# Optimization experiments

Hardware: AMD Instinct MI355X
Metric: run time of the kernel (lower is better)

The kernel has to match this reference:

```python
import jax, jax.numpy as jnp
import numpy as np

D_MODEL = 768
NUM_HEADS = 12
DEPTH = D_MODEL // NUM_HEADS


def setup_inputs() -> dict:
    key = jax.random.key(0)
    ks = jax.random.split(key, 11)
    B, S, D = 2, 2048, D_MODEL
    scale = 1.0 / np.sqrt(D)
    inp = {
        "v": jax.random.normal(ks[0], (B, S, D), jnp.float32),
        "k": jax.random.normal(ks[1], (B, S, D), jnp.float32),
        "q": jax.random.normal(ks[2], (B, S, D), jnp.float32),
        "wq": jax.random.normal(ks[3], (D, D), jnp.float32) * scale,
        "bq": jnp.zeros((D,), jnp.float32),
        "wk": jax.random.normal(ks[4], (D, D), jnp.float32) * scale,
        "bk": jnp.zeros((D,), jnp.float32),
        "wv": jax.random.normal(ks[5], (D, D), jnp.float32) * scale,
        "bv": jnp.zeros((D,), jnp.float32),
        "wo": jax.random.normal(ks[6], (D, D), jnp.float32) * scale,
        "bo": jnp.zeros((D,), jnp.float32),
    }
    return inp


def _split_heads(x):
    # (B, S, D) -> (B, H, S, depth)
    B, S, _ = x.shape
    return x.reshape(B, S, NUM_HEADS, DEPTH).transpose(0, 2, 1, 3)


def reference(v, k, q, wq, bq, wk, bk, wv, bv, wo, bo):
    B, S, D = q.shape
    qh = _split_heads(q @ wq + bq)  # (B,H,S,dh)
    kh = _split_heads(k @ wk + bk)
    vh = _split_heads(v @ wv + bv)
    logits = jnp.einsum("bhqd,bhkd->bhqk", qh, kh) / jnp.sqrt(
        jnp.asarray(DEPTH, qh.dtype)
    )
    attn = jax.nn.softmax(logits, axis=-1)  # (B,H,S,S)
    ctx = jnp.einsum("bhqk,bhkd->bhqd", attn, vh)
    ctx = ctx.transpose(0, 2, 1, 3).reshape(B, S, D)
    return ctx @ wo + bo
```

## Files before the change

kernel.cpp:

```cpp
#include <hip/hip_runtime.h>
#include <hip/hip_bf16.h>
#include <math.h>

typedef __bf16 bf16;
typedef __attribute__((ext_vector_type(8))) __bf16 bf16x8;
typedef __attribute__((ext_vector_type(4))) __bf16 bf16x4v;
typedef __attribute__((ext_vector_type(4))) float f32x4;

#define MFMA16(a, b, c) __builtin_amdgcn_mfma_f32_16x16x32_bf16(a, b, c, 0, 0, 0)

__device__ __forceinline__ void gld16(const bf16* g, bf16* l) {
  __builtin_amdgcn_global_load_lds((const __attribute__((address_space(1))) void*)g,
                                   (__attribute__((address_space(3))) void*)l, 16, 0, 0);
}

__global__ __launch_bounds__(256) void prep(const float* __restrict__ q,
                                            const float* __restrict__ k,
                                            const float* __restrict__ v,
                                            bf16* __restrict__ qb, bf16* __restrict__ kb,
                                            bf16* __restrict__ vb,
                                            const float* __restrict__ w0,
                                            const float* __restrict__ w1,
                                            const float* __restrict__ w2,
                                            const float* __restrict__ w3,
                                            bf16* __restrict__ t0, bf16* __restrict__ t1,
                                            bf16* __restrict__ t2, bf16* __restrict__ t3) {
  const int lin = blockIdx.x;
  if (lin < 4608) {
    const int which = lin / 1536, idx = lin % 1536;
    const float* a = which == 0 ? q : (which == 1 ? k : v);
    bf16* o = which == 0 ? qb : (which == 1 ? kb : vb);
    const size_t i = ((size_t)idx * 256 + threadIdx.x) * 8;
    const float4 f0 = *(const float4*)(a + i);
    const float4 f1 = *(const float4*)(a + i + 4);
    bf16x8 r = {(bf16)f0.x, (bf16)f0.y, (bf16)f0.z, (bf16)f0.w,
                (bf16)f1.x, (bf16)f1.y, (bf16)f1.z, (bf16)f1.w};
    *(bf16x8*)(o + i) = r;
  } else {
    const int w = lin - 4608;
    const int z = w / 576, rem = w % 576;
    const int by = rem / 24, bx = rem % 24;
    const float* W = z == 0 ? w0 : (z == 1 ? w1 : (z == 2 ? w2 : w3));
    bf16* T = z == 0 ? t0 : (z == 1 ? t1 : (z == 2 ? t2 : t3));
    __shared__ float t[32][33];
    const int tx = threadIdx.x & 31, ty = threadIdx.x >> 5;
    const int c0 = bx * 32, r0 = by * 32;
#pragma unroll
    for (int i = 0; i < 4; ++i) {
      const int r = ty + 8 * i;
      t[r][tx] = W[(size_t)(r0 + r) * 768 + c0 + tx];
    }
    __syncthreads();
#pragma unroll
    for (int i = 0; i < 4; ++i) {
      const int r = ty + 8 * i;
      T[(size_t)(c0 + r) * 768 + r0 + tx] = (bf16)t[tx][r];
    }
  }
}

__device__ __forceinline__ void gemm_core(const bf16* __restrict__ A, const bf16* __restrict__ BT,
                                          int row0, int col0, bf16* As, bf16* Bs,
                                          f32x4 acc[4][4]) {
  const int tid = threadIdx.x;
  const int lane = tid & 63, wave = tid >> 6;
  const int m15 = lane & 15, kg = lane >> 4;
  const int wm = wave >> 1, wn = wave & 1;
  const int pr16 = lane & 15;
  const int pk8 = (lane >> 4) * 8;
#pragma unroll
  for (int i = 0; i < 4; ++i)
#pragma unroll
    for (int j = 0; j < 4; ++j) acc[i][j] = f32x4{0.f, 0.f, 0.f, 0.f};

  for (int k0 = 0; k0 < 768; k0 += 32) {
#pragma unroll
    for (int j = 0; j < 2; ++j) {
      const int i = wave * 2 + j;
      gld16(A + (size_t)(row0 + 16 * i + pr16) * 768 + k0 + pk8, As + i * 512);
      gld16(BT + (size_t)(col0 + 16 * i + pr16) * 768 + k0 + pk8, Bs + i * 512);
    }
    __syncthreads();
    bf16x8 af[4], bfr[4];
#pragma unroll
    for (int t = 0; t < 4; ++t)
      af[t] = *(const bf16x8*)(As + (4 * wm + t) * 512 + kg * 128 + m15 * 8);
#pragma unroll
    for (int t = 0; t < 4; ++t)
      bfr[t] = *(const bf16x8*)(Bs + (4 * wn + t) * 512 + kg * 128 + m15 * 8);
#pragma unroll
    for (int mt = 0; mt < 4; ++mt)
#pragma unroll
      for (int nt = 0; nt < 4; ++nt) acc[mt][nt] = MFMA16(af[mt], bfr[nt], acc[mt][nt]);
    __syncthreads();
  }
}

__global__ __launch_bounds__(256, 3) void gemm_qkv(
    const bf16* __restrict__ qb, const bf16* __restrict__ kb, const bf16* __restrict__ vb,
    const bf16* __restrict__ wqT, const bf16* __restrict__ wkT, const bf16* __restrict__ wvT,
    const float* __restrict__ bq, const float* __restrict__ bk, const float* __restrict__ bv,
    bf16* __restrict__ Qh, bf16* __restrict__ Kh, bf16* __restrict__ Vt) {
  __shared__ bf16 As[128 * 32], Bs[128 * 32];
  const bf16 *A, *BT;
  const float* bias;
  bf16* out;
  int mode;
  if (blockIdx.z == 0) { A = qb; BT = wqT; bias = bq; out = Qh; mode = 0; }
  else if (blockIdx.z == 1) { A = kb; BT = wkT; bias = bk; out = Kh; mode = 0; }
  else { A = vb; BT = wvT; bias = bv; out = Vt; mode = 1; }
  const int row0 = blockIdx.y * 128, col0 = blockIdx.x * 128;
  f32x4 acc[4][4];
  gemm_core(A, BT, row0, col0, As, Bs, acc);

  const int lane = threadIdx.x & 63, wave = threadIdx.x >> 6;
  const int m15 = lane & 15, kg = lane >> 4;
  const int wm = wave >> 1, wn = wave & 1;
#pragma unroll
  for (int mt = 0; mt < 4; ++mt) {
#pragma unroll
    for (int nt = 0; nt < 4; ++nt) {
      const int col = col0 + 64 * wn + 16 * nt + m15;
      const float bb = bias[col];
      const int h = col >> 6, d = col & 63;
      const int rowb = row0 + 64 * wm + 16 * mt + kg * 4;
      const int b = rowb >> 11, s0 = rowb & 2047;
      if (mode == 0) {
#pragma unroll
        for (int r = 0; r < 4; ++r)
          out[((size_t)(b * 12 + h) * 2048 + s0 + r) * 64 + d] = (bf16)(acc[mt][nt][r] + bb);
      } else {
        bf16x4v pk;
#pragma unroll
        for (int r = 0; r < 4; ++r) pk[r] = (bf16)(acc[mt][nt][r] + bb);
        *(bf16x4v*)&out[((size_t)(b * 12 + h) * 64 + d) * 2048 + s0] = pk;
      }
    }
  }
}

__global__ __launch_bounds__(256, 3) void gemm_out(const bf16* __restrict__ A,
                                                   const bf16* __restrict__ BT,
                                                   const float* __restrict__ bias,
                                                   float* __restrict__ out) {
  __shared__ bf16 As[64 * 32], Bs[64 * 32];
  const int tid = threadIdx.x;
  const int lane = tid & 63, wave = tid >> 6;
  const int m15 = lane & 15, kg = lane >> 4;
  const int wm = wave >> 1, wn = wave & 1;
  const int row0 = blockIdx.y * 64, col0 = blockIdx.x * 64;
  const int pr16 = lane & 15, pk8 = (lane >> 4) * 8;

  f32x4 acc[2][2];
#pragma unroll
  for (int i = 0; i < 2; ++i)
#pragma unroll
    for (int j = 0; j < 2; ++j) acc[i][j] = f32x4{0.f, 0.f, 0.f, 0.f};

  for (int k0 = 0; k0 < 768; k0 += 32) {
    gld16(A + (size_t)(row0 + 16 * wave + pr16) * 768 + k0 + pk8, As + wave * 512);
    gld16(BT + (size_t)(col0 + 16 * wave + pr16) * 768 + k0 + pk8, Bs + wave * 512);
    __syncthreads();
    bf16x8 af[2], bfr[2];
#pragma unroll
    for (int t = 0; t < 2; ++t)
      af[t] = *(const bf16x8*)(As + (2 * wm + t) * 512 + kg * 128 + m15 * 8);
#pragma unroll
    for (int t = 0; t < 2; ++t)
      bfr[t] = *(const bf16x8*)(Bs + (2 * wn + t) * 512 + kg * 128 + m15 * 8);
#pragma unroll
    for (int mt = 0; mt < 2; ++mt)
#pragma unroll
      for (int nt = 0; nt < 2; ++nt) acc[mt][nt] = MFMA16(af[mt], bfr[nt], acc[mt][nt]);
    __syncthreads();
  }
#pragma unroll
  for (int mt = 0; mt < 2; ++mt) {
#pragma unroll
    for (int nt = 0; nt < 2; ++nt) {
      const int col = col0 + 32 * wn + 16 * nt + m15;
      const float bb = bias[col];
#pragma unroll
      for (int r = 0; r < 4; ++r) {
        const int row = row0 + 32 * wm + 16 * mt + kg * 4 + r;
        out[(size_t)row * 768 + col] = acc[mt][nt][r] + bb;
      }
    }
  }
}

__global__ __launch_bounds__(256, 3) void attn_kernel(const bf16* __restrict__ Q,
                                                      const bf16* __restrict__ K,
                                                      const bf16* __restrict__ VT,
                                                      bf16* __restrict__ ctx) {
  __shared__ __align__(16) bf16 S[21504];

  const int tid = threadIdx.x;
  const int lane = tid & 63, wave = tid >> 6;
  const int m15 = lane & 15, kg = lane >> 4;
  const int lin = blockIdx.x;
  const int bh = lin % 24, qblk = lin / 24;
  const size_t hb = (size_t)bh * 2048 * 64;
  const bf16* Qp = Q + hb;
  const bf16* Kp = K + hb;
  const bf16* Vp = VT + hb;
  const int pipe = wave >> 1;
  const int qrow0 = qblk * 64 + (wave & 1) * 32;
  bf16* Pw = S + 16384 + wave * 1280;

  const int kpr = lane & 7, kpc = (lane >> 3) * 8;
  const int vpr = lane & 15, vpc = (lane >> 4) * 8;

  bf16x8 qf[2][2];
#pragma unroll
  for (int t = 0; t < 2; ++t)
#pragma unroll
    for (int ks = 0; ks < 2; ++ks) {
      bf16x8 tv = *(const bf16x8*)&Qp[(size_t)(qrow0 + 16 * t + m15) * 64 + 32 * ks + kg * 8];
#pragma unroll
      for (int j = 0; j < 8; ++j) tv[j] = (bf16)((float)tv[j] * 0.125f);
      qf[t][ks] = tv;
    }

  f32x4 o[2][4];
  float lp[2][4];
#pragma unroll
  for (int t = 0; t < 2; ++t) {
#pragma unroll
    for (int nt = 0; nt < 4; ++nt) o[t][nt] = f32x4{0.f, 0.f, 0.f, 0.f};
#pragma unroll
    for (int r = 0; r < 4; ++r) lp[t][r] = 0.f;
  }

#pragma unroll
  for (int j = 0; j < 4; ++j) {
    const int idx = wave * 4 + j;
    const int sp = idx >> 3, r8 = idx & 7;
    const int kc = sp * 1024;
    if (r8 < 4)
      gld16(Kp + (size_t)(kc + 8 * r8 + kpr) * 64 + kpc, S + sp * 2 * 2048 + r8 * 512);
    else {
      const int i = r8 - 4;
      gld16(Vp + (size_t)(16 * i + vpr) * 2048 + kc + vpc, S + 8192 + sp * 2 * 2048 + i * 512);
    }
  }

  for (int c = 0; c < 32; ++c) {
    const int buf = c & 1;
    __syncthreads();
    if (c < 31) {
      const int nb = buf ^ 1;
#pragma unroll
      for (int j = 0; j < 4; ++j) {
        const int idx = wave * 4 + j;
        const int sp = idx >> 3, r8 = idx & 7;
        const int kc = sp * 1024 + (c + 1) * 32;
        if (r8 < 4)
          gld16(Kp + (size_t)(kc + 8 * r8 + kpr) * 64 + kpc,
                S + (sp * 2 + nb) * 2048 + r8 * 512);
        else {
          const int i = r8 - 4;
          gld16(Vp + (size_t)(16 * i + vpr) * 2048 + kc + vpc,
                S + 8192 + (sp * 2 + nb) * 2048 + i * 512);
        }
      }
    }
    const bf16* KsB = S + (pipe * 2 + buf) * 2048;
    const bf16* VsB = S + 8192 + (pipe * 2 + buf) * 2048;

    f32x4 s[2][2];
#pragma unroll
    for (int t = 0; t < 2; ++t)
#pragma unroll
      for (int nt = 0; nt < 2; ++nt) s[t][nt] = f32x4{0.f, 0.f, 0.f, 0.f};
#pragma unroll
    for (int ks = 0; ks < 2; ++ks) {
#pragma unroll
      for (int nt = 0; nt < 2; ++nt) {
        const int key = 16 * nt + m15;
        const bf16x8 kf =
            *(const bf16x8*)&KsB[(key >> 3) * 512 + (4 * ks + kg) * 64 + (key & 7) * 8];
        s[0][nt] = MFMA16(qf[0][ks], kf, s[0][nt]);
        s[1][nt] = MFMA16(qf[1][ks], kf, s[1][nt]);
      }
    }
#pragma unroll
    for (int t = 0; t < 2; ++t)
#pragma unroll
      for (int r = 0; r < 4; ++r)
#pragma unroll
        for (int nt = 0; nt < 2; ++nt) {
          const float pe = __expf(s[t][nt][r]);
          lp[t][r] += pe;
          Pw[t * 640 + (kg * 4 + r) * 40 + 16 * nt + m15] = (bf16)pe;
        }
    asm volatile("s_waitcnt lgkmcnt(0)" ::: "memory");
    const bf16x8 pf0 = *(const bf16x8*)&Pw[0 * 640 + m15 * 40 + kg * 8];
    const bf16x8 pf1 = *(const bf16x8*)&Pw[1 * 640 + m15 * 40 + kg * 8];
#pragma unroll
    for (int nt = 0; nt < 4; ++nt) {
      const int d = 16 * nt + m15;
      const bf16x8 vf =
          *(const bf16x8*)&VsB[(d >> 4) * 512 + kg * 128 + (d & 15) * 8];
      o[0][nt] = MFMA16(pf0, vf, o[0][nt]);
      o[1][nt] = MFMA16(pf1, vf, o[1][nt]);
    }
  }

  __syncthreads();
  float* sc = (float*)S;
  if (wave >= 2) {
    const int rg = (wave - 2) * 2560;
#pragma unroll
    for (int t = 0; t < 2; ++t)
#pragma unroll
      for (int nt = 0; nt < 4; ++nt)
        *(f32x4*)&sc[rg + (t * 4 + nt) * 256 + lane * 4] = o[t][nt];
    f32x4 l0 = {lp[0][0], lp[0][1], lp[0][2], lp[0][3]};
    f32x4 l1 = {lp[1][0], lp[1][1], lp[1][2], lp[1][3]};
    *(f32x4*)&sc[rg + 2048 + lane * 8] = l0;
    *(f32x4*)&sc[rg + 2048 + lane * 8 + 4] = l1;
  }
  __syncthreads();
  if (wave < 2) {
    const int rg = wave * 2560;
#pragma unroll
    for (int t = 0; t < 2; ++t)
#pragma unroll
      for (int nt = 0; nt < 4; ++nt) {
        const f32x4 po = *(const f32x4*)&sc[rg + (t * 4 + nt) * 256 + lane * 4];
#pragma unroll
        for (int j = 0; j < 4; ++j) o[t][nt][j] += po[j];
      }
    const f32x4 pl0 = *(const f32x4*)&sc[rg + 2048 + lane * 8];
    const f32x4 pl1 = *(const f32x4*)&sc[rg + 2048 + lane * 8 + 4];
#pragma unroll
    for (int r = 0; r < 4; ++r) { lp[0][r] += pl0[r]; lp[1][r] += pl1[r]; }
#pragma unroll
    for (int t = 0; t < 2; ++t)
#pragma unroll
      for (int r = 0; r < 4; ++r) {
#pragma unroll
        for (int st = 1; st < 16; st <<= 1) lp[t][r] += __shfl_xor(lp[t][r], st);
      }
    const int b = bh / 12, h = bh % 12;
#pragma unroll
    for (int t = 0; t < 2; ++t)
#pragma unroll
      for (int nt = 0; nt < 4; ++nt)
#pragma unroll
        for (int r = 0; r < 4; ++r) {
          const int sr = qrow0 + 16 * t + kg * 4 + r;
          ctx[((size_t)(b * 2048) + sr) * 768 + h * 64 + 16 * nt + m15] =
              (bf16)(o[t][nt][r] / lp[t][r]);
        }
  }
}

extern "C" void kernel_launch(void* const* d_in, const int* in_sizes, int n_in,
                              void* d_out, int out_size, void* d_ws, size_t ws_size,
                              hipStream_t stream) {
  const float* v = (const float*)d_in[0];
  const float* k = (const float*)d_in[1];
  const float* q = (const float*)d_in[2];
  const float* wq = (const float*)d_in[3];
  const float* bq = (const float*)d_in[4];
  const float* wk = (const float*)d_in[5];
  const float* bk = (const float*)d_in[6];
  const float* wv = (const float*)d_in[7];
  const float* bv = (const float*)d_in[8];
  const float* wo = (const float*)d_in[9];
  const float* bo = (const float*)d_in[10];

  char* ws = (char*)d_ws;
  const size_t SEG = (size_t)4096 * 768 * sizeof(bf16);
  const size_t WSEG = (size_t)768 * 768 * sizeof(bf16);
  bf16* Qh = (bf16*)(ws + 0 * SEG);
  bf16* Kh = (bf16*)(ws + 1 * SEG);
  bf16* Vt = (bf16*)(ws + 2 * SEG);
  bf16* qb = (bf16*)(ws + 3 * SEG);
  bf16* kb = (bf16*)(ws + 4 * SEG);
  bf16* vb = (bf16*)(ws + 5 * SEG);
  bf16* ctx = qb;
  bf16* wqT = (bf16*)(ws + 6 * SEG);
  bf16* wkT = (bf16*)(ws + 6 * SEG + WSEG);
  bf16* wvT = (bf16*)(ws + 6 * SEG + 2 * WSEG);
  bf16* woT = (bf16*)(ws + 6 * SEG + 3 * WSEG);

  prep<<<dim3(6912), 256, 0, stream>>>(q, k, v, qb, kb, vb, wq, wk, wv, wo,
                                       wqT, wkT, wvT, woT);
  gemm_qkv<<<dim3(6, 32, 3), 256, 0, stream>>>(qb, kb, vb, wqT, wkT, wvT, bq, bk, bv,
                                               Qh, Kh, Vt);
  attn_kernel<<<dim3(768), 256, 0, stream>>>(Qh, Kh, Vt, ctx);
  gemm_out<<<dim3(12, 64), 256, 0, stream>>>(ctx, woT, bo, (float*)d_out);
}
```

Before: 214.2 us.

## Restructure attention to two waves with direct K/V loads; split-K output GEMM

The attention kernel drops from four waves to two per block. Each wave now handles 64 query rows over half of the keys and loads K and V fragments straight from global memory into registers, replacing the shared-memory double buffering and its per-step barriers. The P tile layout in shared memory changes to match the fragment reads. Separately, the output projection is split along K into two halves that accumulate with atomicAdd after a memset of the output. This raises register pressure and drops LDS reuse of K/V in attention, and adds atomic traffic plus a memset to the output GEMM.

```diff
diff --git a/kernel.cpp b/kernel.cpp
--- a/kernel.cpp
+++ b/kernel.cpp
@@ -149,6 +149,7 @@
   const int m15 = lane & 15, kg = lane >> 4;
   const int wm = wave >> 1, wn = wave & 1;
   const int row0 = blockIdx.y * 64, col0 = blockIdx.x * 64;
+  const int kh = blockIdx.z;
   const int pr16 = lane & 15, pk8 = (lane >> 4) * 8;
 
   f32x4 acc[2][2];
@@ -157,7 +158,7 @@
 #pragma unroll
     for (int j = 0; j < 2; ++j) acc[i][j] = f32x4{0.f, 0.f, 0.f, 0.f};
 
-  for (int k0 = 0; k0 < 768; k0 += 32) {
+  for (int k0 = kh * 384; k0 < kh * 384 + 384; k0 += 32) {
     gld16(A + (size_t)(row0 + 16 * wave + pr16) * 768 + k0 + pk8, As + wave * 512);
     gld16(BT + (size_t)(col0 + 16 * wave + pr16) * 768 + k0 + pk8, Bs + wave * 512);
     __syncthreads();
@@ -179,41 +180,37 @@
 #pragma unroll
     for (int nt = 0; nt < 2; ++nt) {
       const int col = col0 + 32 * wn + 16 * nt + m15;
-      const float bb = bias[col];
+      const float bb = (kh == 0) ? bias[col] : 0.f;
 #pragma unroll
       for (int r = 0; r < 4; ++r) {
         const int row = row0 + 32 * wm + 16 * mt + kg * 4 + r;
-        out[(size_t)row * 768 + col] = acc[mt][nt][r] + bb;
+        atomicAdd(&out[(size_t)row * 768 + col], acc[mt][nt][r] + bb);
       }
     }
   }
 }
 
-__global__ __launch_bounds__(256, 3) void attn_kernel(const bf16* __restrict__ Q,
+__global__ __launch_bounds__(128, 2) void attn_kernel(const bf16* __restrict__ Q,
                                                       const bf16* __restrict__ K,
                                                       const bf16* __restrict__ VT,
                                                       bf16* __restrict__ ctx) {
-  __shared__ __align__(16) bf16 S[21504];
+  __shared__ __align__(16) char SMEM[20480];
 
   const int tid = threadIdx.x;
   const int lane = tid & 63, wave = tid >> 6;
   const int m15 = lane & 15, kg = lane >> 4;
   const int lin = blockIdx.x;
-  const int bh = lin % 24, qblk = lin / 24;
+  const int bh = lin % 24, rg = lin / 24;
   const size_t hb = (size_t)bh * 2048 * 64;
   const bf16* Qp = Q + hb;
   const bf16* Kp = K + hb;
   const bf16* Vp = VT + hb;
-  const int pipe = wave >> 1;
-  const int qrow0 = qblk * 64 + (wave & 1) * 32;
-  bf16* Pw = S + 16384 + wave * 1280;
-
-  const int kpr = lane & 7, kpc = (lane >> 3) * 8;
-  const int vpr = lane & 15, vpc = (lane >> 4) * 8;
-
-  bf16x8 qf[2][2];
-#pragma unroll
-  for (int t = 0; t < 2; ++t)
+  const int qrow0 = rg * 64;
+  bf16* Pw = (bf16*)SMEM + wave * 2048;
+
+  bf16x8 qf[4][2];
+#pragma unroll
+  for (int t = 0; t < 4; ++t)
 #pragma unroll
     for (int ks = 0; ks < 2; ++ks) {
       bf16x8 tv = *(const bf16x8*)&Qp[(size_t)(qrow0 + 16 * t + m15) * 64 + 32 * ks + kg * 8];
@@ -222,122 +219,88 @@
       qf[t][ks] = tv;
     }
 
-  f32x4 o[2][4];
-  float lp[2][4];
-#pragma unroll
-  for (int t = 0; t < 2; ++t) {
+  f32x4 o[4][4];
+  float lp[4][4];
+#pragma unroll
+  for (int t = 0; t < 4; ++t) {
 #pragma unroll
     for (int nt = 0; nt < 4; ++nt) o[t][nt] = f32x4{0.f, 0.f, 0.f, 0.f};
 #pragma unroll
     for (int r = 0; r < 4; ++r) lp[t][r] = 0.f;
   }
 
-#pragma unroll
-  for (int j = 0; j < 4; ++j) {
-    const int idx = wave * 4 + j;
-    const int sp = idx >> 3, r8 = idx & 7;
-    const int kc = sp * 1024;
-    if (r8 < 4)
-      gld16(Kp + (size_t)(kc + 8 * r8 + kpr) * 64 + kpc, S + sp * 2 * 2048 + r8 * 512);
-    else {
-      const int i = r8 - 4;
-      gld16(Vp + (size_t)(16 * i + vpr) * 2048 + kc + vpc, S + 8192 + sp * 2 * 2048 + i * 512);
-    }
-  }
-
+  const int kbase = wave * 1024;
   for (int c = 0; c < 32; ++c) {
-    const int buf = c & 1;
-    __syncthreads();
-    if (c < 31) {
-      const int nb = buf ^ 1;
-#pragma unroll
-      for (int j = 0; j < 4; ++j) {
-        const int idx = wave * 4 + j;
-        const int sp = idx >> 3, r8 = idx & 7;
-        const int kc = sp * 1024 + (c + 1) * 32;
-        if (r8 < 4)
-          gld16(Kp + (size_t)(kc + 8 * r8 + kpr) * 64 + kpc,
-                S + (sp * 2 + nb) * 2048 + r8 * 512);
-        else {
-          const int i = r8 - 4;
-          gld16(Vp + (size_t)(16 * i + vpr) * 2048 + kc + vpc,
-                S + 8192 + (sp * 2 + nb) * 2048 + i * 512);
-        }
-      }
-    }
-    const bf16* KsB = S + (pipe * 2 + buf) * 2048;
-    const bf16* VsB = S + 8192 + (pipe * 2 + buf) * 2048;
-
-    f32x4 s[2][2];
-#pragma unroll
-    for (int t = 0; t < 2; ++t)
+    const int kc = kbase + c * 32;
+    bf16x8 kf[2][2];
+#pragma unroll
+    for (int nt = 0; nt < 2; ++nt)
+#pragma unroll
+      for (int ks = 0; ks < 2; ++ks)
+        kf[nt][ks] = *(const bf16x8*)&Kp[(size_t)(kc + 16 * nt + m15) * 64 + 32 * ks + kg * 8];
+    bf16x8 vf[4];
+#pragma unroll
+    for (int nt = 0; nt < 4; ++nt)
+      vf[nt] = *(const bf16x8*)&Vp[(size_t)(16 * nt + m15) * 2048 + kc + kg * 8];
+    f32x4 s[4][2];
+#pragma unroll
+    for (int t = 0; t < 4; ++t)
 #pragma unroll
       for (int nt = 0; nt < 2; ++nt) s[t][nt] = f32x4{0.f, 0.f, 0.f, 0.f};
 #pragma unroll
-    for (int ks = 0; ks < 2; ++ks) {
-#pragma unroll
-      for (int nt = 0; nt < 2; ++nt) {
-        const int key = 16 * nt + m15;
-        const bf16x8 kf =
-            *(const bf16x8*)&KsB[(key >> 3) * 512 + (4 * ks + kg) * 64 + (key & 7) * 8];
-        s[0][nt] = MFMA16(qf[0][ks], kf, s[0][nt]);
-        s[1][nt] = MFMA16(qf[1][ks], kf, s[1][nt]);
-      }
-    }
-#pragma unroll
-    for (int t = 0; t < 2; ++t)
+    for (int ks = 0; ks < 2; ++ks)
+#pragma unroll
+      for (int nt = 0; nt < 2; ++nt)
+#pragma unroll
+        for (int t = 0; t < 4; ++t) s[t][nt] = MFMA16(qf[t][ks], kf[nt][ks], s[t][nt]);
+#pragma unroll
+    for (int t = 0; t < 4; ++t)
 #pragma unroll
       for (int r = 0; r < 4; ++r)
 #pragma unroll
         for (int nt = 0; nt < 2; ++nt) {
           const float pe = __expf(s[t][nt][r]);
           lp[t][r] += pe;
-          Pw[t * 640 + (kg * 4 + r) * 40 + 16 * nt + m15] = (bf16)pe;
+          const int col = 16 * nt + m15;
+          Pw[t * 512 + (col >> 3) * 128 + (kg * 4 + r) * 8 + (col & 7)] = (bf16)pe;
         }
     asm volatile("s_waitcnt lgkmcnt(0)" ::: "memory");
-    const bf16x8 pf0 = *(const bf16x8*)&Pw[0 * 640 + m15 * 40 + kg * 8];
-    const bf16x8 pf1 = *(const bf16x8*)&Pw[1 * 640 + m15 * 40 + kg * 8];
-#pragma unroll
-    for (int nt = 0; nt < 4; ++nt) {
-      const int d = 16 * nt + m15;
-      const bf16x8 vf =
-          *(const bf16x8*)&VsB[(d >> 4) * 512 + kg * 128 + (d & 15) * 8];
-      o[0][nt] = MFMA16(pf0, vf, o[0][nt]);
-      o[1][nt] = MFMA16(pf1, vf, o[1][nt]);
+#pragma unroll
+    for (int t = 0; t < 4; ++t) {
+      const bf16x8 pf = *(const bf16x8*)&Pw[t * 512 + kg * 128 + m15 * 8];
+#pragma unroll
+      for (int nt = 0; nt < 4; ++nt) o[t][nt] = MFMA16(pf, vf[nt], o[t][nt]);
     }
   }
 
   __syncthreads();
-  float* sc = (float*)S;
-  if (wave >= 2) {
-    const int rg = (wave - 2) * 2560;
-#pragma unroll
-    for (int t = 0; t < 2; ++t)
+  float* sc = (float*)SMEM;
+  if (wave == 1) {
+#pragma unroll
+    for (int t = 0; t < 4; ++t) {
 #pragma unroll
       for (int nt = 0; nt < 4; ++nt)
-        *(f32x4*)&sc[rg + (t * 4 + nt) * 256 + lane * 4] = o[t][nt];
-    f32x4 l0 = {lp[0][0], lp[0][1], lp[0][2], lp[0][3]};
-    f32x4 l1 = {lp[1][0], lp[1][1], lp[1][2], lp[1][3]};
-    *(f32x4*)&sc[rg + 2048 + lane * 8] = l0;
-    *(f32x4*)&sc[rg + 2048 + lane * 8 + 4] = l1;
+        *(f32x4*)&sc[((t * 4 + nt) * 64 + lane) * 4] = o[t][nt];
+      f32x4 l = {lp[t][0], lp[t][1], lp[t][2], lp[t][3]};
+      *(f32x4*)&sc[4096 + (t * 64 + lane) * 4] = l;
+    }
   }
   __syncthreads();
-  if (wave < 2) {
-    const int rg = wave * 2560;
-#pragma unroll
-    for (int t = 0; t < 2; ++t)
+  if (wave == 0) {
+#pragma unroll
+    for (int t = 0; t < 4; ++t) {
 #pragma unroll
       for (int nt = 0; nt < 4; ++nt) {
-        const f32x4 po = *(const f32x4*)&sc[rg + (t * 4 + nt) * 256 + lane * 4];
+        const f32x4 po = *(const f32x4*)&sc[((t * 4 + nt) * 64 + lane) * 4];
 #pragma unroll
         for (int j = 0; j < 4; ++j) o[t][nt][j] += po[j];
       }
-    const f32x4 pl0 = *(const f32x4*)&sc[rg + 2048 + lane * 8];
-    const f32x4 pl1 = *(const f32x4*)&sc[rg + 2048 + lane * 8 + 4];
-#pragma unroll
-    for (int r = 0; r < 4; ++r) { lp[0][r] += pl0[r]; lp[1][r] += pl1[r]; }
-#pragma unroll
-    for (int t = 0; t < 2; ++t)
+      const f32x4 pl = *(const f32x4*)&sc[4096 + (t * 64 + lane) * 4];
+#pragma unroll
+      for (int r = 0; r < 4; ++r) lp[t][r] += pl[r];
+    }
+#pragma unroll
+    for (int t = 0; t < 4; ++t)
 #pragma unroll
       for (int r = 0; r < 4; ++r) {
 #pragma unroll
@@ -345,7 +308,7 @@
       }
     const int b = bh / 12, h = bh % 12;
 #pragma unroll
-    for (int t = 0; t < 2; ++t)
+    for (int t = 0; t < 4; ++t)
 #pragma unroll
       for (int nt = 0; nt < 4; ++nt)
 #pragma unroll
@@ -387,10 +350,12 @@
   bf16* wvT = (bf16*)(ws + 6 * SEG + 2 * WSEG);
   bf16* woT = (bf16*)(ws + 6 * SEG + 3 * WSEG);
 
+  hipMemsetAsync(d_out, 0, (size_t)out_size * sizeof(float), stream);
+
   prep<<<dim3(6912), 256, 0, stream>>>(q, k, v, qb, kb, vb, wq, wk, wv, wo,
                                        wqT, wkT, wvT, woT);
   gemm_qkv<<<dim3(6, 32, 3), 256, 0, stream>>>(qb, kb, vb, wqT, wkT, wvT, bq, bk, bv,
                                                Qh, Kh, Vt);
-  attn_kernel<<<dim3(768), 256, 0, stream>>>(Qh, Kh, Vt, ctx);
-  gemm_out<<<dim3(12, 64), 256, 0, stream>>>(ctx, woT, bo, (float*)d_out);
-}
+  attn_kernel<<<dim3(768), 128, 0, stream>>>(Qh, Kh, Vt, ctx);
+  gemm_out<<<dim3(12, 64, 2), 256, 0, stream>>>(ctx, woT, bo, (float*)d_out);
+}
```

After: 232.6 us. 8.6% more time.
